# Kernel tuning notes

Hardware: AMD Instinct MI355X
Metric: run time of the kernel (lower is better)

Reference implementation:

```python
import jax, jax.numpy as jnp
import numpy as np
from jax import lax

GROUPS = 8
EPS = 1e-5

def setup_inputs() -> dict:
    key = jax.random.key(0)
    ks = jax.random.split(key, 4)
    B, C, H, W = 32, 256, 64, 64
    cg = C // GROUPS  # 32 channels per group
    x = jax.random.normal(ks[0], (B, C, H, W), dtype=jnp.float32)
    w1 = jax.random.normal(ks[1], (cg, cg, 1, 1), dtype=jnp.float32) * 0.02  # conv1x1 OIHW
    b1 = jnp.zeros((cg,), jnp.float32)
    w3 = jax.random.normal(ks[2], (cg, cg, 3, 3), dtype=jnp.float32) * 0.02  # conv3x3 OIHW
    b3 = jnp.zeros((cg,), jnp.float32)
    gn_w = jnp.ones((cg,), jnp.float32)
    gn_b = jnp.zeros((cg,), jnp.float32)
    return {"x": x, "w1": w1, "b1": b1, "w3": w3, "b3": b3, "gn_w": gn_w, "gn_b": gn_b}

def reference(x, w1, b1, w3, b3, gn_w, gn_b):
    B, C, H, W = x.shape
    cg = C // GROUPS
    bg = B * GROUPS
    gx = x.reshape(bg, cg, H, W)

    # coordinate pooling: (bg,cg,H,1) and (bg,cg,W,1)
    x_h = jnp.mean(gx, axis=3, keepdims=True)
    x_w = jnp.mean(gx, axis=2, keepdims=True).transpose(0, 1, 3, 2)

    # 1x1 conv over concatenated coord features (bg,cg,H+W,1)
    hw = jnp.einsum('bihk,oi->bohk', jnp.concatenate([x_h, x_w], axis=2), w1[:, :, 0, 0])
    hw = hw + b1[None, :, None, None]
    xh, xw = hw[:, :, :H, :], hw[:, :, H:, :]

    # sigmoid coordinate gating
    gated = gx * jax.nn.sigmoid(xh) * jax.nn.sigmoid(xw.transpose(0, 1, 3, 2))

    # GroupNorm(cg groups over cg channels) == per-channel instance norm over HxW
    mu = jnp.mean(gated, axis=(2, 3), keepdims=True)
    var = jnp.var(gated, axis=(2, 3), keepdims=True)
    x1 = (gated - mu) * lax.rsqrt(var + EPS)
    x1 = x1 * gn_w[None, :, None, None] + gn_b[None, :, None, None]

    # 3x3 conv branch
    x2 = lax.conv_general_dilated(gx, w3, (1, 1), 'SAME',
                                  dimension_numbers=('NCHW', 'OIHW', 'NCHW'))
    x2 = x2 + b3[None, :, None, None]

    # cross-branch attention weights
    x11 = jax.nn.softmax(jnp.mean(x1, axis=(2, 3)), axis=-1)[:, None, :]  # (bg,1,cg)
    x21 = jax.nn.softmax(jnp.mean(x2, axis=(2, 3)), axis=-1)[:, None, :]  # (bg,1,cg)
    x12 = x2.reshape(bg, cg, H * W)
    x22 = x1.reshape(bg, cg, H * W)
    weights = (jnp.matmul(x11, x12) + jnp.matmul(x21, x22)).reshape(bg, 1, H, W)

    out = (gx * jax.nn.sigmoid(weights)).reshape(B, C, H, W) + x
    return out
```

## Files before the change

kernel.cpp:

```cpp
#include <hip/hip_runtime.h>
#include <math.h>

#define NPLANE 8192
#define PLANE  4096

__device__ __forceinline__ float sigm(float v){ return 1.0f/(1.0f+expf(-v)); }

__global__ __launch_bounds__(256) void kA(const float* __restrict__ x,
                                          float* __restrict__ rowsum,
                                          float* __restrict__ colsum,
                                          float* __restrict__ corners){
  const int plane = blockIdx.x;
  const float* __restrict__ p = x + (size_t)plane*PLANE;
  const int t = threadIdx.x;
  __shared__ float cpart[256][5];
  __shared__ float rsh[64];
  float4 v[4];
  #pragma unroll
  for(int it=0; it<4; ++it)
    v[it] = *reinterpret_cast<const float4*>(p + it*1024 + t*4);
  if(t==0)   corners[(size_t)plane*4+0]=v[0].x;
  if(t==15)  corners[(size_t)plane*4+1]=v[0].w;
  if(t==240) corners[(size_t)plane*4+2]=v[3].x;
  if(t==255) corners[(size_t)plane*4+3]=v[3].w;
  float ca0=0.f, ca1=0.f, ca2=0.f, ca3=0.f;
  #pragma unroll
  for(int it=0; it<4; ++it){
    float rp = v[it].x+v[it].y+v[it].z+v[it].w;
    #pragma unroll
    for(int s=1;s<16;s<<=1) rp += __shfl_xor(rp, s, 64);
    if((t&15)==0) rsh[it*16 + (t>>4)] = rp;
    ca0+=v[it].x; ca1+=v[it].y; ca2+=v[it].z; ca3+=v[it].w;
  }
  cpart[t][0]=ca0; cpart[t][1]=ca1; cpart[t][2]=ca2; cpart[t][3]=ca3;
  __syncthreads();
  if(t<64){
    const int g=t>>2, j=t&3;
    float s=0.f;
    #pragma unroll
    for(int k=0;k<16;++k) s += cpart[g + k*16][j];
    colsum[(size_t)plane*64 + t] = s;
    rowsum[(size_t)plane*64 + t] = rsh[t];
  }
}

__global__ __launch_bounds__(256) void kB0(const float* __restrict__ gn_b,
                                           const float* __restrict__ w3,
                                           const float* __restrict__ b3,
                                           float* __restrict__ wcg,
                                           float* __restrict__ cbg){
  __shared__ float x11[32];
  const int t=threadIdx.x;
  if(t==0){
    float m=-1e30f;
    #pragma unroll
    for(int c=0;c<32;++c) m=fmaxf(m,gn_b[c]);
    float e[32]; float s=0.f;
    #pragma unroll
    for(int c=0;c<32;++c){ e[c]=expf(gn_b[c]-m); s+=e[c]; }
    const float inv=1.f/s;
    float cb=0.f;
    #pragma unroll
    for(int c=0;c<32;++c){ x11[c]=e[c]*inv; cb+=x11[c]*b3[c]; }
    *cbg=cb;
  }
  __syncthreads();
  for(int idx=t; idx<288; idx+=256){
    const int i=idx/9, k=idx%9;
    float s=0.f;
    #pragma unroll
    for(int c=0;c<32;++c) s += x11[c]*w3[(c*32+i)*9+k];
    wcg[idx]=s;
  }
}

__global__ __launch_bounds__(256) void kB(const float* __restrict__ rowsum,
                                          const float* __restrict__ colsum,
                                          const float* __restrict__ corners,
                                          const float* __restrict__ w1,
                                          const float* __restrict__ b1,
                                          const float* __restrict__ w3,
                                          const float* __restrict__ b3,
                                          float* __restrict__ sh,
                                          float* __restrict__ sw,
                                          float* __restrict__ x21){
  const int b = blockIdx.x;
  const int t = threadIdx.x;
  __shared__ float m[32*132];
  __shared__ float w1t[1024];
  __shared__ float w3t[9216];
  __shared__ float sout[32*132];
  __shared__ float S[288];
  __shared__ float red[256];
  const float* __restrict__ rs = rowsum + (size_t)b*2048;
  const float* __restrict__ cs = colsum + (size_t)b*2048;
  for(int idx=t; idx<2048; idx+=256){
    const int i=idx>>6, h=idx&63;
    m[i*132+h]    = rs[idx]*(1.0f/64.0f);
    m[i*132+64+h] = cs[idx]*(1.0f/64.0f);
  }
  for(int idx=t; idx<1024; idx+=256) w1t[idx] = w1[(idx&31)*32 + (idx>>5)];
  for(int idx=t; idx<9216; idx+=256){
    const int c=idx&31, r=idx>>5, i=r/9, k=r-9*i;
    w3t[idx] = w3[(c*32+i)*9+k];
  }
  __syncthreads();
  {
    const int o = t&31, pg = t>>5;
    const float bo = b1[o];
    #pragma unroll
    for(int pp=0;pp<16;++pp){
      const int p = pg*16+pp;
      float a = bo;
      #pragma unroll
      for(int i=0;i<32;++i) a += w1t[i*32+o]*m[i*132+p];
      sout[o*132+p] = sigm(a);
    }
  }
  if(t<32){
    const int i=t;
    float Ti=0.f;
    for(int h=0;h<64;++h) Ti += m[i*132+h];
    Ti *= 64.f;
    const float r0=m[i*132+0]*64.f, r63=m[i*132+63]*64.f;
    const float c0=m[i*132+64]*64.f, c63=m[i*132+127]*64.f;
    const float* cr = corners + ((size_t)b*32+i)*4;
    const float k00=cr[0], k01=cr[1], k10=cr[2], k11=cr[3];
    #pragma unroll
    for(int ky=0;ky<3;++ky){
      #pragma unroll
      for(int kx=0;kx<3;++kx){
        float s=Ti;
        if(ky==0) s-=r63; else if(ky==2) s-=r0;
        if(kx==0) s-=c63; else if(kx==2) s-=c0;
        if(ky==0&&kx==0) s+=k11;
        if(ky==0&&kx==2) s+=k10;
        if(ky==2&&kx==0) s+=k01;
        if(ky==2&&kx==2) s+=k00;
        S[i*9+ky*3+kx]=s;
      }
    }
  }
  __syncthreads();
  {
    const int c = t&31, chunk = t>>5;
    float part = 0.f;
    #pragma unroll
    for(int ii=0; ii<4; ++ii){
      const int i = chunk*4+ii;
      #pragma unroll
      for(int k=0;k<9;++k) part += w3t[(i*9+k)*32+c]*S[i*9+k];
    }
    red[t] = part;
  }
  __syncthreads();
  if(t<32){
    float mm=0.f;
    #pragma unroll
    for(int ch=0;ch<8;++ch) mm += red[ch*32+t];
    mm = mm*(1.0f/4096.0f) + b3[t];
    float mx = mm;
    #pragma unroll
    for(int s=1;s<32;s<<=1) mx = fmaxf(mx, __shfl_xor(mx,s,64));
    const float e = expf(mm-mx);
    float ss = e;
    #pragma unroll
    for(int s=1;s<32;s<<=1) ss += __shfl_xor(ss,s,64);
    x21[(size_t)b*32+t] = e/ss;
  }
  for(int idx=t; idx<2048; idx+=256){
    sh[(size_t)b*2048+idx] = sout[(idx>>6)*132 + (idx&63)];
    sw[(size_t)b*2048+idx] = sout[(idx>>6)*132 + 64 + (idx&63)];
  }
}

__global__ __launch_bounds__(256) void kC(const float* __restrict__ x,
                                          const float* __restrict__ sh,
                                          const float* __restrict__ sw,
                                          float* __restrict__ musum,
                                          float* __restrict__ sqsum){
  const int plane = blockIdx.x;
  const int t = threadIdx.x;
  const float* __restrict__ p = x + (size_t)plane*PLANE;
  __shared__ float shs[64], sws[64];
  float4 v[4];
  #pragma unroll
  for(int it=0;it<4;++it)
    v[it] = *reinterpret_cast<const float4*>(p + it*1024 + t*4);
  if(t<64){ shs[t]=sh[(size_t)plane*64+t]; sws[t]=sw[(size_t)plane*64+t]; }
  __syncthreads();
  const int col = (t&15)<<2;
  const float4 swv = *reinterpret_cast<const float4*>(&sws[col]);
  float s=0.f, q=0.f;
  #pragma unroll
  for(int it=0;it<4;++it){
    const float a = shs[it*16 + (t>>4)];
    const float g0=v[it].x*a*swv.x, g1=v[it].y*a*swv.y;
    const float g2=v[it].z*a*swv.z, g3=v[it].w*a*swv.w;
    s += g0+g1+g2+g3;
    q += g0*g0+g1*g1+g2*g2+g3*g3;
  }
  #pragma unroll
  for(int sft=1;sft<64;sft<<=1){ s+=__shfl_xor(s,sft,64); q+=__shfl_xor(q,sft,64); }
  __shared__ float rsum[4], rsq[4];
  if((t&63)==0){ rsum[t>>6]=s; rsq[t>>6]=q; }
  __syncthreads();
  if(t==0){ musum[plane]=rsum[0]+rsum[1]+rsum[2]+rsum[3];
            sqsum[plane]=rsq[0]+rsq[1]+rsq[2]+rsq[3]; }
}

#define TEB 320
__global__ __launch_bounds__(TEB) void kE(const float* __restrict__ x,
    const float* __restrict__ sh, const float* __restrict__ sw,
    const float* __restrict__ x21, const float* __restrict__ musum,
    const float* __restrict__ sqsum, const float* __restrict__ gn_w,
    const float* __restrict__ gn_b, const float* __restrict__ wc,
    const float* __restrict__ cb, float* __restrict__ out){
  const int b = blockIdx.x>>2;
  const int tile0 = (blockIdx.x&3)<<4;
  const int t = threadIdx.x;
  __shared__ float H[3*18*68];
  __shared__ float sws[32*64];
  __shared__ float shs[32*16];
  __shared__ float alphas[32];
  __shared__ float wcs[292];
  __shared__ float constsh;

  if(t<32){
    const float ms = musum[(size_t)b*32+t]*(1.0f/4096.0f);
    const float vv = sqsum[(size_t)b*32+t]*(1.0f/4096.0f) - ms*ms;
    const float rq = rsqrtf(vv + 1e-5f);
    const float xv = x21[(size_t)b*32+t];
    alphas[t] = xv*gn_w[t]*rq;
    float part = xv*(gn_b[t] - gn_w[t]*rq*ms);
    #pragma unroll
    for(int s=1;s<32;s<<=1) part += __shfl_xor(part, s, 64);
    if(t==0) constsh = part + cb[0];
  }
  for(int idx=t; idx<288; idx+=TEB) wcs[idx]=wc[idx];
  for(int idx=t; idx<512; idx+=TEB)
    shs[idx] = sh[(size_t)b*2048 + (idx>>4)*64 + tile0 + (idx&15)];
  for(int idx=t; idx<2048; idx+=TEB)
    sws[idx] = sw[(size_t)b*2048 + idx];
  __syncthreads();

  const int hr = t>>4;
  const int c0 = (t&15)<<2;
  const int gr = tile0 + hr - 1;
  float acc[4][9];
  float gacc[4];

  if(t < 288){
    #pragma unroll
    for(int j=0;j<4;++j){
      gacc[j]=0.f;
      #pragma unroll
      for(int k=0;k<9;++k) acc[j][k]=0.f;
    }
    const float rowmask = (hr>=1 && hr<=16) ? 1.f : 0.f;
    const int   shi = min(max(hr-1,0),15);
    const bool  inrow = (gr>=0) && (gr<64);
    const float* __restrict__ px = x + ((size_t)b*32)*PLANE + (size_t)gr*64 + c0;
    #pragma unroll 2
    for(int i=0;i<32;++i){
      float4 v = make_float4(0.f,0.f,0.f,0.f);
      if(inrow) v = *reinterpret_cast<const float4*>(px + (size_t)i*PLANE);
      const float ash = alphas[i]*shs[i*16+shi]*rowmask;
      const float4 swv = *reinterpret_cast<const float4*>(&sws[i*64+c0]);
      const float* __restrict__ wq = &wcs[i*9];
      const float vv0=v.x, vv1=v.y, vv2=v.z, vv3=v.w;
      #pragma unroll
      for(int k=0;k<9;++k){
        const float w = wq[k];
        acc[0][k] += w*vv0; acc[1][k] += w*vv1;
        acc[2][k] += w*vv2; acc[3][k] += w*vv3;
      }
      gacc[0] += ash*swv.x*vv0; gacc[1] += ash*swv.y*vv1;
      gacc[2] += ash*swv.z*vv2; gacc[3] += ash*swv.w*vv3;
    }
    #pragma unroll
    for(int ky=0;ky<3;++ky){
      float lf = __shfl_up(acc[3][ky*3+0], 1);
      float rt = __shfl_down(acc[0][ky*3+2], 1);
      if(c0==0)  lf = 0.f;
      if(c0==60) rt = 0.f;
      const float h0 = lf             + acc[0][ky*3+1] + acc[1][ky*3+2];
      const float h1 = acc[0][ky*3+0] + acc[1][ky*3+1] + acc[2][ky*3+2];
      const float h2 = acc[1][ky*3+0] + acc[2][ky*3+1] + acc[3][ky*3+2];
      const float h3 = acc[2][ky*3+0] + acc[3][ky*3+1] + rt;
      *reinterpret_cast<float4*>(&H[(ky*18+hr)*68 + c0]) = make_float4(h0,h1,h2,h3);
    }
  }
  __syncthreads();
  if(t>=16 && t<272){
    const float4 h0 = *reinterpret_cast<const float4*>(&H[(0*18 + hr-1)*68 + c0]);
    const float4 h1 = *reinterpret_cast<const float4*>(&H[(1*18 + hr  )*68 + c0]);
    const float4 h2 = *reinterpret_cast<const float4*>(&H[(2*18 + hr+1)*68 + c0]);
    const float cst = constsh;
    const float wf0 = 1.f + sigm(h0.x+h1.x+h2.x + gacc[0] + cst);
    const float wf1 = 1.f + sigm(h0.y+h1.y+h2.y + gacc[1] + cst);
    const float wf2 = 1.f + sigm(h0.z+h1.z+h2.z + gacc[2] + cst);
    const float wf3 = 1.f + sigm(h0.w+h1.w+h2.w + gacc[3] + cst);
    const float* __restrict__ px = x   + ((size_t)b*32)*PLANE + (size_t)gr*64 + c0;
    float*       __restrict__ po = out + ((size_t)b*32)*PLANE + (size_t)gr*64 + c0;
    #pragma unroll 4
    for(int i=0;i<32;++i){
      const float4 v = *reinterpret_cast<const float4*>(px + (size_t)i*PLANE);
      float4 o;
      o.x=v.x*wf0; o.y=v.y*wf1; o.z=v.z*wf2; o.w=v.w*wf3;
      *reinterpret_cast<float4*>(po + (size_t)i*PLANE) = o;
    }
  }
}

extern "C" void kernel_launch(void* const* d_in, const int* in_sizes, int n_in,
                              void* d_out, int out_size, void* d_ws, size_t ws_size,
                              hipStream_t stream){
  (void)in_sizes; (void)n_in; (void)out_size; (void)ws_size;
  const float* x    = (const float*)d_in[0];
  const float* w1   = (const float*)d_in[1];
  const float* b1   = (const float*)d_in[2];
  const float* w3   = (const float*)d_in[3];
  const float* b3   = (const float*)d_in[4];
  const float* gn_w = (const float*)d_in[5];
  const float* gn_b = (const float*)d_in[6];
  float* out = (float*)d_out;
  float* ws  = (float*)d_ws;

  float* rowsum  = ws + 0;
  float* colsum  = ws + 524288;
  float* corners = ws + 1048576;
  float* sh      = ws + 1081344;
  float* sw      = ws + 1605632;
  float* x21     = ws + 2129920;
  float* musum   = ws + 2138112;
  float* sqsum   = ws + 2146304;
  float* wc      = ws + 2154496;
  float* cb      = ws + 2154784;

  kA <<<NPLANE, 256, 0, stream>>>(x, rowsum, colsum, corners);
  kB0<<<1,      256, 0, stream>>>(gn_b, w3, b3, wc, cb);
  kB <<<256,    256, 0, stream>>>(rowsum, colsum, corners, w1, b1, w3, b3, sh, sw, x21);
  kC <<<NPLANE, 256, 0, stream>>>(x, sh, sw, musum, sqsum);
  kE <<<1024,   TEB, 0, stream>>>(x, sh, sw, x21, musum, sqsum, gn_w, gn_b, wc, cb, out);
}
```

Before: 343.6 us.

## Fuse pooling, stats, attention and output into one per-group kernel

Replaces the five-kernel pipeline with a small weight-prep kernel plus one fused kernel. The fused kernel uses one 1024-thread block per batch-group and does all of its work there: row and column marginals, the sigmoid gates, the GroupNorm statistics, the conv-mean softmax, and the full-plane 3x3 conv with sigmoid output. This removes the global round-trips for row and column sums, gates and statistics, and cuts kernel launches. In exchange the grid has only 256 large blocks, which limits occupancy and latency hiding. The block's x slice is still read several times, so the design relies on cache reuse.

```diff
diff --git a/kernel.cpp b/kernel.cpp
--- a/kernel.cpp
+++ b/kernel.cpp
@@ -1,54 +1,15 @@
 #include <hip/hip_runtime.h>
 #include <math.h>
 
-#define NPLANE 8192
-#define PLANE  4096
+#define PLANE 4096
 
 __device__ __forceinline__ float sigm(float v){ return 1.0f/(1.0f+expf(-v)); }
 
-__global__ __launch_bounds__(256) void kA(const float* __restrict__ x,
-                                          float* __restrict__ rowsum,
-                                          float* __restrict__ colsum,
-                                          float* __restrict__ corners){
-  const int plane = blockIdx.x;
-  const float* __restrict__ p = x + (size_t)plane*PLANE;
-  const int t = threadIdx.x;
-  __shared__ float cpart[256][5];
-  __shared__ float rsh[64];
-  float4 v[4];
-  #pragma unroll
-  for(int it=0; it<4; ++it)
-    v[it] = *reinterpret_cast<const float4*>(p + it*1024 + t*4);
-  if(t==0)   corners[(size_t)plane*4+0]=v[0].x;
-  if(t==15)  corners[(size_t)plane*4+1]=v[0].w;
-  if(t==240) corners[(size_t)plane*4+2]=v[3].x;
-  if(t==255) corners[(size_t)plane*4+3]=v[3].w;
-  float ca0=0.f, ca1=0.f, ca2=0.f, ca3=0.f;
-  #pragma unroll
-  for(int it=0; it<4; ++it){
-    float rp = v[it].x+v[it].y+v[it].z+v[it].w;
-    #pragma unroll
-    for(int s=1;s<16;s<<=1) rp += __shfl_xor(rp, s, 64);
-    if((t&15)==0) rsh[it*16 + (t>>4)] = rp;
-    ca0+=v[it].x; ca1+=v[it].y; ca2+=v[it].z; ca3+=v[it].w;
-  }
-  cpart[t][0]=ca0; cpart[t][1]=ca1; cpart[t][2]=ca2; cpart[t][3]=ca3;
-  __syncthreads();
-  if(t<64){
-    const int g=t>>2, j=t&3;
-    float s=0.f;
-    #pragma unroll
-    for(int k=0;k<16;++k) s += cpart[g + k*16][j];
-    colsum[(size_t)plane*64 + t] = s;
-    rowsum[(size_t)plane*64 + t] = rsh[t];
-  }
-}
-
-__global__ __launch_bounds__(256) void kB0(const float* __restrict__ gn_b,
-                                           const float* __restrict__ w3,
-                                           const float* __restrict__ b3,
-                                           float* __restrict__ wcg,
-                                           float* __restrict__ cbg){
+__global__ __launch_bounds__(256) void kPrep(const float* __restrict__ gn_b,
+    const float* __restrict__ w1, const float* __restrict__ w3,
+    const float* __restrict__ b3,
+    float* __restrict__ wcg, float* __restrict__ cbg,
+    float* __restrict__ w1T, float* __restrict__ w3T){
   __shared__ float x11[32];
   const int t=threadIdx.x;
   if(t==0){
@@ -72,202 +33,206 @@
     for(int c=0;c<32;++c) s += x11[c]*w3[(c*32+i)*9+k];
     wcg[idx]=s;
   }
+  for(int idx=t; idx<1024; idx+=256) w1T[idx] = w1[(idx&31)*32 + (idx>>5)];
+  for(int idx=t; idx<9216; idx+=256){
+    const int c=idx&31, r=idx>>5, i=r/9, k=r-9*i;
+    w3T[idx] = w3[(c*32+i)*9+k];
+  }
 }
 
-__global__ __launch_bounds__(256) void kB(const float* __restrict__ rowsum,
-                                          const float* __restrict__ colsum,
-                                          const float* __restrict__ corners,
-                                          const float* __restrict__ w1,
-                                          const float* __restrict__ b1,
-                                          const float* __restrict__ w3,
-                                          const float* __restrict__ b3,
-                                          float* __restrict__ sh,
-                                          float* __restrict__ sw,
-                                          float* __restrict__ x21){
+#define TB 1024
+__global__ __launch_bounds__(TB, 4) void kFused(const float* __restrict__ x,
+    const float* __restrict__ b1, const float* __restrict__ b3,
+    const float* __restrict__ gn_w, const float* __restrict__ gn_b,
+    const float* __restrict__ wc, const float* __restrict__ cb,
+    const float* __restrict__ w1T, const float* __restrict__ w3T,
+    float* __restrict__ out){
   const int b = blockIdx.x;
   const int t = threadIdx.x;
-  __shared__ float m[32*132];
-  __shared__ float w1t[1024];
-  __shared__ float w3t[9216];
-  __shared__ float sout[32*132];
-  __shared__ float S[288];
-  __shared__ float red[256];
-  const float* __restrict__ rs = rowsum + (size_t)b*2048;
-  const float* __restrict__ cs = colsum + (size_t)b*2048;
-  for(int idx=t; idx<2048; idx+=256){
-    const int i=idx>>6, h=idx&63;
-    m[i*132+h]    = rs[idx]*(1.0f/64.0f);
-    m[i*132+64+h] = cs[idx]*(1.0f/64.0f);
-  }
-  for(int idx=t; idx<1024; idx+=256) w1t[idx] = w1[(idx&31)*32 + (idx>>5)];
-  for(int idx=t; idx<9216; idx+=256){
-    const int c=idx&31, r=idx>>5, i=r/9, k=r-9*i;
-    w3t[idx] = w3[(c*32+i)*9+k];
-  }
-  __syncthreads();
-  {
-    const int o = t&31, pg = t>>5;
+  __shared__ float L[15936];
+  float* SW   = L;
+  float* WCS  = L+2048;
+  float* ALPH = L+2336;
+  float* MUS  = L+2400;
+  float* SQS  = L+2432;
+  float* CST  = L+2464;
+  float* MARG = L+2468;
+  float* W1S  = L+6692;
+  float* S    = L+7716;
+  float* CORN = L+8004;
+  float* SH   = L+8132;
+  float* Hb   = L+2468;
+
+  const float* __restrict__ xb = x + (size_t)b*32*PLANE;
+
+  for(int idx=t; idx<288; idx+=TB) WCS[idx]=wc[idx];
+  for(int idx=t; idx<1024; idx+=TB) W1S[idx]=w1T[idx];
+
+  {
+    const int i = t>>5, j = t&31;
+    const float* __restrict__ p = xb + (size_t)i*PLANE + j*4;
+    float ca0=0.f, ca1=0.f, ca2=0.f, ca3=0.f;
+    #pragma unroll
+    for(int ch=0; ch<4; ++ch){
+      float4 v[8];
+      #pragma unroll
+      for(int k=0;k<8;++k) v[k] = *reinterpret_cast<const float4*>(p + (ch*8+k)*128);
+      #pragma unroll
+      for(int k=0;k<8;++k){
+        const int s = ch*8+k;
+        float rp = v[k].x+v[k].y+v[k].z+v[k].w;
+        rp += __shfl_xor(rp,1,64); rp += __shfl_xor(rp,2,64);
+        rp += __shfl_xor(rp,4,64); rp += __shfl_xor(rp,8,64);
+        if((j&15)==0) MARG[i*132 + 2*s + (j>>4)] = rp;
+        ca0+=v[k].x; ca1+=v[k].y; ca2+=v[k].z; ca3+=v[k].w;
+        if(ch==0&&k==0){ if(j==0)  CORN[i*4+0]=v[k].x;
+                         if(j==15) CORN[i*4+1]=v[k].w; }
+        if(ch==3&&k==7){ if(j==16) CORN[i*4+2]=v[k].x;
+                         if(j==31) CORN[i*4+3]=v[k].w; }
+      }
+    }
+    ca0+=__shfl_xor(ca0,16,64); ca1+=__shfl_xor(ca1,16,64);
+    ca2+=__shfl_xor(ca2,16,64); ca3+=__shfl_xor(ca3,16,64);
+    if(j<16) *reinterpret_cast<float4*>(&MARG[i*132+64+4*j]) =
+        make_float4(ca0,ca1,ca2,ca3);
+  }
+  __syncthreads();
+
+  {
+    const int o = t>>5;
+    const int p0 = (t&31)*4;
+    float a0=0.f,a1=0.f,a2=0.f,a3=0.f;
+    #pragma unroll
+    for(int i=0;i<32;++i){
+      const float w = W1S[i*32+o];
+      const float4 mv = *reinterpret_cast<const float4*>(&MARG[i*132+p0]);
+      a0+=w*mv.x; a1+=w*mv.y; a2+=w*mv.z; a3+=w*mv.w;
+    }
     const float bo = b1[o];
-    #pragma unroll
-    for(int pp=0;pp<16;++pp){
-      const int p = pg*16+pp;
-      float a = bo;
-      #pragma unroll
-      for(int i=0;i<32;++i) a += w1t[i*32+o]*m[i*132+p];
-      sout[o*132+p] = sigm(a);
-    }
-  }
-  if(t<32){
-    const int i=t;
-    float Ti=0.f;
-    for(int h=0;h<64;++h) Ti += m[i*132+h];
-    Ti *= 64.f;
-    const float r0=m[i*132+0]*64.f, r63=m[i*132+63]*64.f;
-    const float c0=m[i*132+64]*64.f, c63=m[i*132+127]*64.f;
-    const float* cr = corners + ((size_t)b*32+i)*4;
-    const float k00=cr[0], k01=cr[1], k10=cr[2], k11=cr[3];
-    #pragma unroll
-    for(int ky=0;ky<3;++ky){
-      #pragma unroll
-      for(int kx=0;kx<3;++kx){
-        float s=Ti;
-        if(ky==0) s-=r63; else if(ky==2) s-=r0;
-        if(kx==0) s-=c63; else if(kx==2) s-=c0;
-        if(ky==0&&kx==0) s+=k11;
-        if(ky==0&&kx==2) s+=k10;
-        if(ky==2&&kx==0) s+=k01;
-        if(ky==2&&kx==2) s+=k00;
-        S[i*9+ky*3+kx]=s;
+    const float inv64 = 1.0f/64.0f;
+    float4 r;
+    r.x=sigm(bo+a0*inv64); r.y=sigm(bo+a1*inv64);
+    r.z=sigm(bo+a2*inv64); r.w=sigm(bo+a3*inv64);
+    if(p0<64) *reinterpret_cast<float4*>(&SH[o*64+p0])      = r;
+    else      *reinterpret_cast<float4*>(&SW[o*64+p0-64])   = r;
+  }
+  __syncthreads();
+
+  {
+    const int i = t>>5, j = t&31;
+    const float* __restrict__ p = xb + (size_t)i*PLANE + j*4;
+    const float4 swv = *reinterpret_cast<const float4*>(&SW[i*64+(j&15)*4]);
+    float s=0.f, q=0.f;
+    #pragma unroll
+    for(int ch=0; ch<4; ++ch){
+      float4 v[8];
+      #pragma unroll
+      for(int k=0;k<8;++k) v[k] = *reinterpret_cast<const float4*>(p + (ch*8+k)*128);
+      #pragma unroll
+      for(int k=0;k<8;++k){
+        const int srow = 2*(ch*8+k) + (j>>4);
+        const float a = SH[i*64+srow];
+        const float g0=v[k].x*a*swv.x, g1=v[k].y*a*swv.y;
+        const float g2=v[k].z*a*swv.z, g3=v[k].w*a*swv.w;
+        s += g0+g1+g2+g3;
+        q += g0*g0+g1*g1+g2*g2+g3*g3;
       }
     }
-  }
-  __syncthreads();
-  {
+    s+=__shfl_xor(s,1,64); s+=__shfl_xor(s,2,64); s+=__shfl_xor(s,4,64);
+    s+=__shfl_xor(s,8,64); s+=__shfl_xor(s,16,64);
+    q+=__shfl_xor(q,1,64); q+=__shfl_xor(q,2,64); q+=__shfl_xor(q,4,64);
+    q+=__shfl_xor(q,8,64); q+=__shfl_xor(q,16,64);
+    if(j==0){ MUS[i]=s; SQS[i]=q; }
+    if(t<32){
+      const int ii=t;
+      float Ti=0.f;
+      for(int h=0;h<64;++h) Ti += MARG[ii*132+h];
+      const float r0=MARG[ii*132+0],  r63=MARG[ii*132+63];
+      const float c0s=MARG[ii*132+64], c63s=MARG[ii*132+127];
+      const float k00=CORN[ii*4+0], k01=CORN[ii*4+1];
+      const float k10=CORN[ii*4+2], k11=CORN[ii*4+3];
+      #pragma unroll
+      for(int ky=0;ky<3;++ky){
+        #pragma unroll
+        for(int kx=0;kx<3;++kx){
+          float ss=Ti;
+          if(ky==0) ss-=r63; else if(ky==2) ss-=r0;
+          if(kx==0) ss-=c63s; else if(kx==2) ss-=c0s;
+          if(ky==0&&kx==0) ss+=k11;
+          if(ky==0&&kx==2) ss+=k10;
+          if(ky==2&&kx==0) ss+=k01;
+          if(ky==2&&kx==2) ss+=k00;
+          S[ii*9+ky*3+kx]=ss;
+        }
+      }
+    }
+  }
+  __syncthreads();
+
+  if(t<256){
     const int c = t&31, chunk = t>>5;
     float part = 0.f;
     #pragma unroll
     for(int ii=0; ii<4; ++ii){
       const int i = chunk*4+ii;
       #pragma unroll
-      for(int k=0;k<9;++k) part += w3t[(i*9+k)*32+c]*S[i*9+k];
-    }
-    red[t] = part;
+      for(int k=0;k<9;++k) part += w3T[(i*9+k)*32+c]*S[i*9+k];
+    }
+    W1S[t] = part;
   }
   __syncthreads();
   if(t<32){
     float mm=0.f;
     #pragma unroll
-    for(int ch=0;ch<8;++ch) mm += red[ch*32+t];
+    for(int ch=0;ch<8;++ch) mm += W1S[ch*32+t];
     mm = mm*(1.0f/4096.0f) + b3[t];
     float mx = mm;
     #pragma unroll
-    for(int s=1;s<32;s<<=1) mx = fmaxf(mx, __shfl_xor(mx,s,64));
+    for(int s2=1;s2<32;s2<<=1) mx = fmaxf(mx, __shfl_xor(mx,s2,64));
     const float e = expf(mm-mx);
     float ss = e;
     #pragma unroll
-    for(int s=1;s<32;s<<=1) ss += __shfl_xor(ss,s,64);
-    x21[(size_t)b*32+t] = e/ss;
-  }
-  for(int idx=t; idx<2048; idx+=256){
-    sh[(size_t)b*2048+idx] = sout[(idx>>6)*132 + (idx&63)];
-    sw[(size_t)b*2048+idx] = sout[(idx>>6)*132 + 64 + (idx&63)];
-  }
-}
-
-__global__ __launch_bounds__(256) void kC(const float* __restrict__ x,
-                                          const float* __restrict__ sh,
-                                          const float* __restrict__ sw,
-                                          float* __restrict__ musum,
-                                          float* __restrict__ sqsum){
-  const int plane = blockIdx.x;
-  const int t = threadIdx.x;
-  const float* __restrict__ p = x + (size_t)plane*PLANE;
-  __shared__ float shs[64], sws[64];
-  float4 v[4];
+    for(int s2=1;s2<32;s2<<=1) ss += __shfl_xor(ss,s2,64);
+    const float xv = e/ss;
+    const float ms = MUS[t]*(1.0f/4096.0f);
+    const float vv = SQS[t]*(1.0f/4096.0f) - ms*ms;
+    const float rq = rsqrtf(vv + 1e-5f);
+    ALPH[t] = xv*gn_w[t]*rq;
+    float part2 = xv*(gn_b[t] - gn_w[t]*rq*ms);
+    #pragma unroll
+    for(int s2=1;s2<32;s2<<=1) part2 += __shfl_xor(part2,s2,64);
+    if(t==0) CST[0] = part2 + cb[0];
+  }
+  __syncthreads();
+
+  const int row = t>>4;
+  const int c0  = (t&15)<<2;
+  float ashr[32];
   #pragma unroll
-  for(int it=0;it<4;++it)
-    v[it] = *reinterpret_cast<const float4*>(p + it*1024 + t*4);
-  if(t<64){ shs[t]=sh[(size_t)plane*64+t]; sws[t]=sw[(size_t)plane*64+t]; }
-  __syncthreads();
-  const int col = (t&15)<<2;
-  const float4 swv = *reinterpret_cast<const float4*>(&sws[col]);
-  float s=0.f, q=0.f;
-  #pragma unroll
-  for(int it=0;it<4;++it){
-    const float a = shs[it*16 + (t>>4)];
-    const float g0=v[it].x*a*swv.x, g1=v[it].y*a*swv.y;
-    const float g2=v[it].z*a*swv.z, g3=v[it].w*a*swv.w;
-    s += g0+g1+g2+g3;
-    q += g0*g0+g1*g1+g2*g2+g3*g3;
-  }
-  #pragma unroll
-  for(int sft=1;sft<64;sft<<=1){ s+=__shfl_xor(s,sft,64); q+=__shfl_xor(q,sft,64); }
-  __shared__ float rsum[4], rsq[4];
-  if((t&63)==0){ rsum[t>>6]=s; rsq[t>>6]=q; }
-  __syncthreads();
-  if(t==0){ musum[plane]=rsum[0]+rsum[1]+rsum[2]+rsum[3];
-            sqsum[plane]=rsq[0]+rsq[1]+rsq[2]+rsq[3]; }
-}
-
-#define TEB 320
-__global__ __launch_bounds__(TEB) void kE(const float* __restrict__ x,
-    const float* __restrict__ sh, const float* __restrict__ sw,
-    const float* __restrict__ x21, const float* __restrict__ musum,
-    const float* __restrict__ sqsum, const float* __restrict__ gn_w,
-    const float* __restrict__ gn_b, const float* __restrict__ wc,
-    const float* __restrict__ cb, float* __restrict__ out){
-  const int b = blockIdx.x>>2;
-  const int tile0 = (blockIdx.x&3)<<4;
-  const int t = threadIdx.x;
-  __shared__ float H[3*18*68];
-  __shared__ float sws[32*64];
-  __shared__ float shs[32*16];
-  __shared__ float alphas[32];
-  __shared__ float wcs[292];
-  __shared__ float constsh;
-
-  if(t<32){
-    const float ms = musum[(size_t)b*32+t]*(1.0f/4096.0f);
-    const float vv = sqsum[(size_t)b*32+t]*(1.0f/4096.0f) - ms*ms;
-    const float rq = rsqrtf(vv + 1e-5f);
-    const float xv = x21[(size_t)b*32+t];
-    alphas[t] = xv*gn_w[t]*rq;
-    float part = xv*(gn_b[t] - gn_w[t]*rq*ms);
-    #pragma unroll
-    for(int s=1;s<32;s<<=1) part += __shfl_xor(part, s, 64);
-    if(t==0) constsh = part + cb[0];
-  }
-  for(int idx=t; idx<288; idx+=TEB) wcs[idx]=wc[idx];
-  for(int idx=t; idx<512; idx+=TEB)
-    shs[idx] = sh[(size_t)b*2048 + (idx>>4)*64 + tile0 + (idx&15)];
-  for(int idx=t; idx<2048; idx+=TEB)
-    sws[idx] = sw[(size_t)b*2048 + idx];
-  __syncthreads();
-
-  const int hr = t>>4;
-  const int c0 = (t&15)<<2;
-  const int gr = tile0 + hr - 1;
+  for(int i=0;i<32;++i) ashr[i] = ALPH[i]*SH[i*64+row];
+  __syncthreads();
+
+  if(t<102){
+    const int m=t/34, rr=((t%34)/17)*65, cc=(t%17)*4;
+    *reinterpret_cast<float4*>(&Hb[m*4488 + rr*68 + cc]) = make_float4(0.f,0.f,0.f,0.f);
+  }
+
   float acc[4][9];
   float gacc[4];
-
-  if(t < 288){
-    #pragma unroll
-    for(int j=0;j<4;++j){
-      gacc[j]=0.f;
-      #pragma unroll
-      for(int k=0;k<9;++k) acc[j][k]=0.f;
-    }
-    const float rowmask = (hr>=1 && hr<=16) ? 1.f : 0.f;
-    const int   shi = min(max(hr-1,0),15);
-    const bool  inrow = (gr>=0) && (gr<64);
-    const float* __restrict__ px = x + ((size_t)b*32)*PLANE + (size_t)gr*64 + c0;
-    #pragma unroll 2
+  #pragma unroll
+  for(int jj=0;jj<4;++jj){
+    gacc[jj]=0.f;
+    #pragma unroll
+    for(int k=0;k<9;++k) acc[jj][k]=0.f;
+  }
+  {
+    const float* __restrict__ px = xb + row*64 + c0;
+    #pragma unroll 4
     for(int i=0;i<32;++i){
-      float4 v = make_float4(0.f,0.f,0.f,0.f);
-      if(inrow) v = *reinterpret_cast<const float4*>(px + (size_t)i*PLANE);
-      const float ash = alphas[i]*shs[i*16+shi]*rowmask;
-      const float4 swv = *reinterpret_cast<const float4*>(&sws[i*64+c0]);
-      const float* __restrict__ wq = &wcs[i*9];
+      const float4 v = *reinterpret_cast<const float4*>(px + (size_t)i*PLANE);
+      const float4 swv = *reinterpret_cast<const float4*>(&SW[i*64+c0]);
+      const float* __restrict__ wq = &WCS[i*9];
+      const float ash = ashr[i];
       const float vv0=v.x, vv1=v.y, vv2=v.z, vv3=v.w;
       #pragma unroll
       for(int k=0;k<9;++k){
@@ -278,31 +243,33 @@
       gacc[0] += ash*swv.x*vv0; gacc[1] += ash*swv.y*vv1;
       gacc[2] += ash*swv.z*vv2; gacc[3] += ash*swv.w*vv3;
     }
-    #pragma unroll
-    for(int ky=0;ky<3;++ky){
-      float lf = __shfl_up(acc[3][ky*3+0], 1);
-      float rt = __shfl_down(acc[0][ky*3+2], 1);
-      if(c0==0)  lf = 0.f;
-      if(c0==60) rt = 0.f;
-      const float h0 = lf             + acc[0][ky*3+1] + acc[1][ky*3+2];
-      const float h1 = acc[0][ky*3+0] + acc[1][ky*3+1] + acc[2][ky*3+2];
-      const float h2 = acc[1][ky*3+0] + acc[2][ky*3+1] + acc[3][ky*3+2];
-      const float h3 = acc[2][ky*3+0] + acc[3][ky*3+1] + rt;
-      *reinterpret_cast<float4*>(&H[(ky*18+hr)*68 + c0]) = make_float4(h0,h1,h2,h3);
-    }
-  }
-  __syncthreads();
-  if(t>=16 && t<272){
-    const float4 h0 = *reinterpret_cast<const float4*>(&H[(0*18 + hr-1)*68 + c0]);
-    const float4 h1 = *reinterpret_cast<const float4*>(&H[(1*18 + hr  )*68 + c0]);
-    const float4 h2 = *reinterpret_cast<const float4*>(&H[(2*18 + hr+1)*68 + c0]);
-    const float cst = constsh;
+  }
+  #pragma unroll
+  for(int ky=0;ky<3;++ky){
+    float lf = __shfl_up(acc[3][ky*3+0], 1);
+    float rt = __shfl_down(acc[0][ky*3+2], 1);
+    if(c0==0)  lf = 0.f;
+    if(c0==60) rt = 0.f;
+    const float h0 = lf             + acc[0][ky*3+1] + acc[1][ky*3+2];
+    const float h1 = acc[0][ky*3+0] + acc[1][ky*3+1] + acc[2][ky*3+2];
+    const float h2 = acc[1][ky*3+0] + acc[2][ky*3+1] + acc[3][ky*3+2];
+    const float h3 = acc[2][ky*3+0] + acc[3][ky*3+1] + rt;
+    *reinterpret_cast<float4*>(&Hb[ky*4488 + (row+1)*68 + c0]) =
+        make_float4(h0,h1,h2,h3);
+  }
+  __syncthreads();
+
+  {
+    const float4 h0 = *reinterpret_cast<const float4*>(&Hb[0*4488 + (row  )*68 + c0]);
+    const float4 h1 = *reinterpret_cast<const float4*>(&Hb[1*4488 + (row+1)*68 + c0]);
+    const float4 h2 = *reinterpret_cast<const float4*>(&Hb[2*4488 + (row+2)*68 + c0]);
+    const float cst = CST[0];
     const float wf0 = 1.f + sigm(h0.x+h1.x+h2.x + gacc[0] + cst);
     const float wf1 = 1.f + sigm(h0.y+h1.y+h2.y + gacc[1] + cst);
     const float wf2 = 1.f + sigm(h0.z+h1.z+h2.z + gacc[2] + cst);
     const float wf3 = 1.f + sigm(h0.w+h1.w+h2.w + gacc[3] + cst);
-    const float* __restrict__ px = x   + ((size_t)b*32)*PLANE + (size_t)gr*64 + c0;
-    float*       __restrict__ po = out + ((size_t)b*32)*PLANE + (size_t)gr*64 + c0;
+    const float* __restrict__ px = xb + row*64 + c0;
+    float*       __restrict__ po = out + (size_t)b*32*PLANE + row*64 + c0;
     #pragma unroll 4
     for(int i=0;i<32;++i){
       const float4 v = *reinterpret_cast<const float4*>(px + (size_t)i*PLANE);
@@ -327,20 +294,11 @@
   float* out = (float*)d_out;
   float* ws  = (float*)d_ws;
 
-  float* rowsum  = ws + 0;
-  float* colsum  = ws + 524288;
-  float* corners = ws + 1048576;
-  float* sh      = ws + 1081344;
-  float* sw      = ws + 1605632;
-  float* x21     = ws + 2129920;
-  float* musum   = ws + 2138112;
-  float* sqsum   = ws + 2146304;
-  float* wc      = ws + 2154496;
-  float* cb      = ws + 2154784;
-
-  kA <<<NPLANE, 256, 0, stream>>>(x, rowsum, colsum, corners);
-  kB0<<<1,      256, 0, stream>>>(gn_b, w3, b3, wc, cb);
-  kB <<<256,    256, 0, stream>>>(rowsum, colsum, corners, w1, b1, w3, b3, sh, sw, x21);
-  kC <<<NPLANE, 256, 0, stream>>>(x, sh, sw, musum, sqsum);
-  kE <<<1024,   TEB, 0, stream>>>(x, sh, sw, x21, musum, sqsum, gn_w, gn_b, wc, cb, out);
+  float* wc  = ws + 0;
+  float* cb  = ws + 288;
+  float* w1T = ws + 320;
+  float* w3T = ws + 1344;
+
+  kPrep <<<1,   256, 0, stream>>>(gn_b, w1, w3, b3, wc, cb, w1T, w3T);
+  kFused<<<256, TB,  0, stream>>>(x, b1, b3, gn_w, gn_b, wc, cb, w1T, w3T, out);
 }
```

New measurement: 352.6 us. 1.03x slower.
